# Performance work log

Measured on AMD Instinct MI355X. Metric: run time of the kernel, lower is better.

Reference implementation:

```python
import jax, jax.numpy as jnp
import numpy as np
import math

B, S, D, NPOS = 8, 2048, 768, 512


def setup_inputs() -> dict:
    key = jax.random.key(0)
    ks = jax.random.split(key, 9)
    std = 0.02
    return {
        "token_embeddings": jax.random.normal(ks[0], (B, S, D), dtype=jnp.float32),
        "attention_mask": jnp.ones((B, S), dtype=jnp.int32),
        "Wq": jax.random.normal(ks[1], (D, D), dtype=jnp.float32) * std,
        "bq": jax.random.normal(ks[2], (D,), dtype=jnp.float32) * std,
        "Wk": jax.random.normal(ks[3], (D, D), dtype=jnp.float32) * std,
        "bk": jax.random.normal(ks[4], (D,), dtype=jnp.float32) * std,
        "Wv": jax.random.normal(ks[5], (D, D), dtype=jnp.float32) * std,
        "bv": jax.random.normal(ks[6], (D,), dtype=jnp.float32) * std,
        "pos_emb": jax.random.normal(ks[7], (D, NPOS), dtype=jnp.float32) * std,
    }


def reference(token_embeddings, attention_mask, Wq, bq, Wk, bk, Wv, bv, pos_emb):
    scale = 1.0 / math.sqrt(D)
    q = token_embeddings @ Wq.T + bq  # [B,S,D]
    k = token_embeddings @ Wk.T + bk
    v = token_embeddings @ Wv.T + bv

    logits = jnp.einsum("bsd,btd->bst", q, k) * scale  # [B,S,S]
    logits = jnp.where(attention_mask[:, None, :] == 0, -jnp.inf, logits)

    # CoPE: gate-based fractional positions + interpolated learned bias
    gates = jax.nn.sigmoid(logits)
    pos = jnp.flip(jnp.cumsum(jnp.flip(gates, -1), axis=-1), -1)  # reverse cumsum
    pos = jnp.minimum(pos, float(NPOS - 1))
    pos_floor = jnp.floor(pos)
    pos_ceil = jnp.ceil(pos)
    logits_int = jnp.einsum("bsd,dn->bsn", q, pos_emb)  # [B,S,NPOS]
    lc = jnp.take_along_axis(logits_int, pos_ceil.astype(jnp.int32), axis=-1)
    lf = jnp.take_along_axis(logits_int, pos_floor.astype(jnp.int32), axis=-1)
    w = pos - pos_floor
    logits = logits + lc * w + lf * (1.0 - w)

    attn = jax.nn.softmax(logits, axis=-1)
    out = jnp.einsum("bst,btd->bsd", attn, v)
    return out[:, 0, :]  # CLS pooled sentence embedding [B,D]
```

## Files before the change

kernel.cpp:

```cpp
#include <hip/hip_runtime.h>
#include <hip/hip_bf16.h>
#include <math.h>

#define BB 8
#define SS 2048
#define DD 768
#define NPOS 512
#define TC 64
#define DSPLIT 16
#define DSL (DD / DSPLIT)
#define ETOT (DD + NPOS)
#define SCALE 0.036084391824351615f

#define WS_LOGITS 0
#define WS_CTX    16384
#define WS_Q      22528
#define WS_PWS    28672
#define WS_PWQ    192512

__device__ __forceinline__ float wave_sum(float v) {
    #pragma unroll
    for (int off = 32; off > 0; off >>= 1) v += __shfl_xor(v, off, 64);
    return v;
}

__global__ __launch_bounds__(256) void k_q(const float* __restrict__ x,
        const float* __restrict__ Wq, const float* __restrict__ bq,
        float* __restrict__ q, float* __restrict__ ctx) {
    int zi = blockIdx.x * 256 + threadIdx.x;
    if (zi < BB * DD) ctx[zi] = 0.f;
    int gw = zi >> 6;
    int lane = threadIdx.x & 63;
    if (gw >= BB * DD) return;
    int b = gw / DD, d = gw % DD;
    const float4* vr = (const float4*)(x + (size_t)b * SS * DD);
    const float4* wr = (const float4*)(Wq + (size_t)d * DD);
    float acc = 0.f;
    #pragma unroll
    for (int j = 0; j < 3; ++j) {
        float4 a = vr[lane + 64 * j];
        float4 w = wr[lane + 64 * j];
        acc += a.x * w.x + a.y * w.y + a.z * w.z + a.w * w.w;
    }
    acc = wave_sum(acc);
    if (lane == 0) q[gw] = acc + bq[d];
}

__global__ __launch_bounds__(256) void k_qkw(const float* __restrict__ q,
        const float* __restrict__ Wk, const float* __restrict__ bk,
        const float* __restrict__ pos_emb,
        float* __restrict__ pws, float* __restrict__ pwq) {
    int part = blockIdx.x, ds = blockIdx.y, tid = threadIdx.x;
    __shared__ float qs[BB][DSL];
    for (int i = tid; i < BB * DSL; i += 256) {
        int b = i / DSL, d = i % DSL;
        qs[b][d] = q[b * DD + ds * DSL + d];
    }
    __syncthreads();
    const float* Wsrc; int stride, eg;
    if (part < 3) { Wsrc = Wk; stride = DD; eg = part * 256 + tid; }
    else { Wsrc = pos_emb; stride = NPOS; eg = DD + (part - 3) * 256 + tid; }
    int e = (part < 3) ? eg : eg - DD;
    const float* col = Wsrc + (size_t)(ds * DSL) * stride + e;
    float acc[BB];
    #pragma unroll
    for (int b = 0; b < BB; ++b) acc[b] = 0.f;
    #pragma unroll 4
    for (int d = 0; d < DSL; ++d) {
        float w = col[(size_t)d * stride];
        #pragma unroll
        for (int b = 0; b < BB; ++b) acc[b] += qs[b][d] * w;
    }
    #pragma unroll
    for (int b = 0; b < BB; ++b)
        pws[((size_t)ds * BB + b) * ETOT + eg] = acc[b];
    if (part == 0 && tid < BB) {
        float p = 0.f;
        #pragma unroll
        for (int d = 0; d < DSL; ++d) p += qs[tid][d] * bk[ds * DSL + d];
        pwq[ds * BB + tid] = p;
    }
}

__global__ __launch_bounds__(1024) void k_logits(const float* __restrict__ x,
        const float* __restrict__ pws, const float* __restrict__ pwq,
        const int* __restrict__ mask, float* __restrict__ logits) {
    const int chunk = blockIdx.x, b = blockIdx.y, tid = threadIdx.x;
    const int lane = tid & 63, wid = tid >> 6;
    __shared__ float sq[4][192];
    __shared__ float sqbk;
    if (tid < DD) {
        float acc = 0.f;
        #pragma unroll 4
        for (int ds = 0; ds < DSPLIT; ++ds)
            acc += pws[((size_t)ds * BB + b) * ETOT + tid];
        sq[tid & 3][tid >> 2] = acc;
    }
    if (wid == 15) {
        float p = (lane < DSPLIT) ? pwq[lane * BB + b] : 0.f;
        p = wave_sum(p);
        if (lane == 0) sqbk = p;
    }
    __syncthreads();
    #pragma unroll 2
    for (int r = 0; r < 8; ++r) {
        int trow = chunk * 128 + wid * 8 + r;
        const float4* xr = (const float4*)(x + ((size_t)b * SS + trow) * DD);
        float acc = 0.f;
        #pragma unroll
        for (int j = 0; j < 3; ++j) {
            int i = lane + 64 * j;
            float4 a = xr[i];
            acc += a.x * sq[0][i] + a.y * sq[1][i] + a.z * sq[2][i] + a.w * sq[3][i];
        }
        acc = wave_sum(acc);
        if (lane == 0) {
            int o = b * SS + trow;
            logits[o] = mask[o] ? (acc + sqbk) * SCALE : -INFINITY;
        }
    }
}

__global__ __launch_bounds__(256) void k_ctxscan(const float* __restrict__ x,
        const float* __restrict__ logits, const float* __restrict__ pws,
        float* __restrict__ ctx) {
    const int tc = blockIdx.x, b = blockIdx.y, tid = threadIdx.x;
    __shared__ float lg[SS];
    __shared__ float li[NPOS];
    __shared__ float sa[256], sb[256];
    for (int i = tid; i < SS; i += 256) lg[i] = logits[b * SS + i];
    for (int e = tid; e < NPOS; e += 256) {
        float acc = 0.f;
        #pragma unroll 4
        for (int ds = 0; ds < DSPLIT; ++ds)
            acc += pws[((size_t)ds * BB + b) * ETOT + DD + e];
        li[e] = acc;
    }
    __syncthreads();
    int base = tid * 8;
    float loc[8];
    float run = 0.f;
    #pragma unroll
    for (int k = 7; k >= 0; --k) {
        float v = lg[base + k];
        float gk = 1.f / (1.f + expf(-v));
        run += gk;
        loc[k] = run;
    }
    sa[tid] = run;
    __syncthreads();
    float* src = sa; float* dst = sb;
    for (int off = 1; off < 256; off <<= 1) {
        float v = src[tid];
        if (tid + off < 256) v += src[tid + off];
        dst[tid] = v;
        __syncthreads();
        float* t_ = src; src = dst; dst = t_;
    }
    float st = (tid < 255) ? src[tid + 1] : 0.f;
    float adj[8];
    float m = -INFINITY;
    #pragma unroll
    for (int k = 0; k < 8; ++k) {
        float val = lg[base + k];
        float nv;
        if (val == -INFINITY) {
            nv = val;
        } else {
            float p = fminf(loc[k] + st, (float)(NPOS - 1));
            float pf = floorf(p);
            float wt = p - pf;
            int fi = (int)pf;
            int ci = (int)ceilf(p);
            nv = val + li[ci] * wt + li[fi] * (1.f - wt);
        }
        adj[k] = nv;
        m = fmaxf(m, nv);
    }
    __syncthreads();
    sa[tid] = m;
    __syncthreads();
    for (int s2 = 128; s2 > 0; s2 >>= 1) {
        if (tid < s2) sa[tid] = fmaxf(sa[tid], sa[tid + s2]);
        __syncthreads();
    }
    float bm = sa[0];
    __syncthreads();
    float sum = 0.f;
    #pragma unroll
    for (int k = 0; k < 8; ++k) { adj[k] = expf(adj[k] - bm); sum += adj[k]; }
    sa[tid] = sum;
    __syncthreads();
    for (int s2 = 128; s2 > 0; s2 >>= 1) {
        if (tid < s2) sa[tid] += sa[tid + s2];
        __syncthreads();
    }
    float inv = 1.f / sa[0];
    #pragma unroll
    for (int k = 0; k < 8; ++k) lg[base + k] = adj[k] * inv;
    __syncthreads();
    if (tid < 192) {
        const int TPC = SS / TC;
        float4 acc = make_float4(0.f, 0.f, 0.f, 0.f);
        const float4* xr = (const float4*)(x + ((size_t)b * SS + (size_t)tc * TPC) * DD);
        const float* at = lg + tc * TPC;
        for (int i = 0; i < TPC; ++i) {
            float a = at[i];
            float4 xv = xr[(size_t)i * 192 + tid];
            acc.x += a * xv.x; acc.y += a * xv.y; acc.z += a * xv.z; acc.w += a * xv.w;
        }
        float* dstp = ctx + b * DD + tid * 4;
        atomicAdd(dstp + 0, acc.x);
        atomicAdd(dstp + 1, acc.y);
        atomicAdd(dstp + 2, acc.z);
        atomicAdd(dstp + 3, acc.w);
    }
}

__global__ __launch_bounds__(256) void k_out(const float* __restrict__ ctx,
        const float* __restrict__ Wv, const float* __restrict__ bv,
        float* __restrict__ out) {
    int gw = (blockIdx.x * 256 + threadIdx.x) >> 6;
    int lane = threadIdx.x & 63;
    if (gw >= BB * DD) return;
    int b = gw / DD, d = gw % DD;
    const float4* vr = (const float4*)(ctx + (size_t)b * DD);
    const float4* wr = (const float4*)(Wv + (size_t)d * DD);
    float acc = 0.f;
    #pragma unroll
    for (int j = 0; j < 3; ++j) {
        float4 a = vr[lane + 64 * j];
        float4 w = wr[lane + 64 * j];
        acc += a.x * w.x + a.y * w.y + a.z * w.z + a.w * w.w;
    }
    acc = wave_sum(acc);
    if (lane == 0) out[gw] = acc + bv[d];
}

extern "C" void kernel_launch(void* const* d_in, const int* in_sizes, int n_in,
                              void* d_out, int out_size, void* d_ws, size_t ws_size,
                              hipStream_t stream) {
    const float* x       = (const float*)d_in[0];
    const int*   mask    = (const int*)  d_in[1];
    const float* Wq      = (const float*)d_in[2];
    const float* bq      = (const float*)d_in[3];
    const float* Wk      = (const float*)d_in[4];
    const float* bk      = (const float*)d_in[5];
    const float* Wv      = (const float*)d_in[6];
    const float* bv      = (const float*)d_in[7];
    const float* pos_emb = (const float*)d_in[8];
    float* out = (float*)d_out;
    float* ws  = (float*)d_ws;

    float* logits = ws + WS_LOGITS;
    float* ctx    = ws + WS_CTX;
    float* q      = ws + WS_Q;
    float* pws    = ws + WS_PWS;
    float* pwq    = ws + WS_PWQ;

    k_q<<<dim3((BB * DD) / 4), dim3(256), 0, stream>>>(x, Wq, bq, q, ctx);
    k_qkw<<<dim3(5, DSPLIT), dim3(256), 0, stream>>>(q, Wk, bk, pos_emb, pws, pwq);
    k_logits<<<dim3(16, BB), dim3(1024), 0, stream>>>(x, pws, pwq, mask, logits);
    k_ctxscan<<<dim3(TC, BB), dim3(256), 0, stream>>>(x, logits, pws, ctx);
    k_out<<<dim3((BB * DD) / 4), dim3(256), 0, stream>>>(ctx, Wv, bv, out);
}
```

Baseline: 53.90 us.

## Split partial-sum reduction into separate kernel and flatten logits to one wave per row

Adds a small reduction kernel that sums the DSPLIT partial products once into qk and positional-logit buffers. Previously every logits block and every ctxscan block re-reduced them. k_logits now uses 256-thread blocks with one wave per token row across 4096 blocks, instead of 128 blocks of 1024 threads each looping over 8 rows. The q·bk bias term is now computed in a single block. The cost is one extra kernel launch and a round trip through global memory.

```diff
diff --git a/kernel.cpp b/kernel.cpp
--- a/kernel.cpp
+++ b/kernel.cpp
@@ -15,8 +15,10 @@
 #define WS_LOGITS 0
 #define WS_CTX    16384
 #define WS_Q      22528
-#define WS_PWS    28672
-#define WS_PWQ    192512
+#define WS_QK     28672
+#define WS_LI     34816
+#define WS_QBK    38912
+#define WS_PWS    38928
 
 __device__ __forceinline__ float wave_sum(float v) {
     #pragma unroll
@@ -49,7 +51,7 @@
 __global__ __launch_bounds__(256) void k_qkw(const float* __restrict__ q,
         const float* __restrict__ Wk, const float* __restrict__ bk,
         const float* __restrict__ pos_emb,
-        float* __restrict__ pws, float* __restrict__ pwq) {
+        float* __restrict__ pws, float* __restrict__ qbk) {
     int part = blockIdx.x, ds = blockIdx.y, tid = threadIdx.x;
     __shared__ float qs[BB][DSL];
     for (int i = tid; i < BB * DSL; i += 256) {
@@ -74,68 +76,66 @@
     #pragma unroll
     for (int b = 0; b < BB; ++b)
         pws[((size_t)ds * BB + b) * ETOT + eg] = acc[b];
-    if (part == 0 && tid < BB) {
-        float p = 0.f;
+    if (part == 0 && ds == 0) {
+        int w = tid >> 6, lane = tid & 63;
         #pragma unroll
-        for (int d = 0; d < DSL; ++d) p += qs[tid][d] * bk[ds * DSL + d];
-        pwq[ds * BB + tid] = p;
-    }
-}
-
-__global__ __launch_bounds__(1024) void k_logits(const float* __restrict__ x,
-        const float* __restrict__ pws, const float* __restrict__ pwq,
+        for (int r = 0; r < 2; ++r) {
+            int b = w + 4 * r;
+            float p = 0.f;
+            #pragma unroll
+            for (int j = 0; j < 12; ++j)
+                p += q[b * DD + lane + 64 * j] * bk[lane + 64 * j];
+            p = wave_sum(p);
+            if (lane == 0) qbk[b] = p;
+        }
+    }
+}
+
+__global__ __launch_bounds__(256) void k_qkr(const float* __restrict__ pws,
+        float* __restrict__ qk, float* __restrict__ lint) {
+    int idx = blockIdx.x * 256 + threadIdx.x;
+    if (idx >= BB * ETOT) return;
+    int b = idx / ETOT, e = idx % ETOT;
+    float acc = 0.f;
+    #pragma unroll
+    for (int ds = 0; ds < DSPLIT; ++ds)
+        acc += pws[((size_t)ds * BB + b) * ETOT + e];
+    if (e < DD) qk[b * DD + e] = acc;
+    else lint[b * NPOS + (e - DD)] = acc;
+}
+
+__global__ __launch_bounds__(256) void k_logits(const float* __restrict__ x,
+        const float* __restrict__ qk, const float* __restrict__ qbk,
         const int* __restrict__ mask, float* __restrict__ logits) {
-    const int chunk = blockIdx.x, b = blockIdx.y, tid = threadIdx.x;
-    const int lane = tid & 63, wid = tid >> 6;
-    __shared__ float sq[4][192];
-    __shared__ float sqbk;
-    if (tid < DD) {
-        float acc = 0.f;
-        #pragma unroll 4
-        for (int ds = 0; ds < DSPLIT; ++ds)
-            acc += pws[((size_t)ds * BB + b) * ETOT + tid];
-        sq[tid & 3][tid >> 2] = acc;
-    }
-    if (wid == 15) {
-        float p = (lane < DSPLIT) ? pwq[lane * BB + b] : 0.f;
-        p = wave_sum(p);
-        if (lane == 0) sqbk = p;
-    }
-    __syncthreads();
-    #pragma unroll 2
-    for (int r = 0; r < 8; ++r) {
-        int trow = chunk * 128 + wid * 8 + r;
-        const float4* xr = (const float4*)(x + ((size_t)b * SS + trow) * DD);
-        float acc = 0.f;
-        #pragma unroll
-        for (int j = 0; j < 3; ++j) {
-            int i = lane + 64 * j;
-            float4 a = xr[i];
-            acc += a.x * sq[0][i] + a.y * sq[1][i] + a.z * sq[2][i] + a.w * sq[3][i];
-        }
-        acc = wave_sum(acc);
-        if (lane == 0) {
-            int o = b * SS + trow;
-            logits[o] = mask[o] ? (acc + sqbk) * SCALE : -INFINITY;
-        }
+    int gw = (blockIdx.x * 256 + threadIdx.x) >> 6;
+    int lane = threadIdx.x & 63;
+    if (gw >= BB * SS) return;
+    int b = gw >> 11;
+    const float4* xr = (const float4*)(x + (size_t)gw * DD);
+    const float4* wr = (const float4*)(qk + (size_t)b * DD);
+    float acc = 0.f;
+    #pragma unroll
+    for (int j = 0; j < 3; ++j) {
+        float4 a = xr[lane + 64 * j];
+        float4 w = wr[lane + 64 * j];
+        acc += a.x * w.x + a.y * w.y + a.z * w.z + a.w * w.w;
+    }
+    acc = wave_sum(acc);
+    if (lane == 0) {
+        float lg = (acc + qbk[b]) * SCALE;
+        logits[gw] = mask[gw] ? lg : -INFINITY;
     }
 }
 
 __global__ __launch_bounds__(256) void k_ctxscan(const float* __restrict__ x,
-        const float* __restrict__ logits, const float* __restrict__ pws,
+        const float* __restrict__ logits, const float* __restrict__ lint,
         float* __restrict__ ctx) {
     const int tc = blockIdx.x, b = blockIdx.y, tid = threadIdx.x;
     __shared__ float lg[SS];
     __shared__ float li[NPOS];
     __shared__ float sa[256], sb[256];
     for (int i = tid; i < SS; i += 256) lg[i] = logits[b * SS + i];
-    for (int e = tid; e < NPOS; e += 256) {
-        float acc = 0.f;
-        #pragma unroll 4
-        for (int ds = 0; ds < DSPLIT; ++ds)
-            acc += pws[((size_t)ds * BB + b) * ETOT + DD + e];
-        li[e] = acc;
-    }
+    for (int i = tid; i < NPOS; i += 256) li[i] = lint[b * NPOS + i];
     __syncthreads();
     int base = tid * 8;
     float loc[8];
@@ -255,12 +255,15 @@
     float* logits = ws + WS_LOGITS;
     float* ctx    = ws + WS_CTX;
     float* q      = ws + WS_Q;
+    float* qk     = ws + WS_QK;
+    float* lint   = ws + WS_LI;
+    float* qbk    = ws + WS_QBK;
     float* pws    = ws + WS_PWS;
-    float* pwq    = ws + WS_PWQ;
 
     k_q<<<dim3((BB * DD) / 4), dim3(256), 0, stream>>>(x, Wq, bq, q, ctx);
-    k_qkw<<<dim3(5, DSPLIT), dim3(256), 0, stream>>>(q, Wk, bk, pos_emb, pws, pwq);
-    k_logits<<<dim3(16, BB), dim3(1024), 0, stream>>>(x, pws, pwq, mask, logits);
-    k_ctxscan<<<dim3(TC, BB), dim3(256), 0, stream>>>(x, logits, pws, ctx);
+    k_qkw<<<dim3(5, DSPLIT), dim3(256), 0, stream>>>(q, Wk, bk, pos_emb, pws, qbk);
+    k_qkr<<<dim3(40), dim3(256), 0, stream>>>(pws, qk, lint);
+    k_logits<<<dim3((BB * SS) / 4), dim3(256), 0, stream>>>(x, qk, qbk, mask, logits);
+    k_ctxscan<<<dim3(TC, BB), dim3(256), 0, stream>>>(x, logits, lint, ctx);
     k_out<<<dim3((BB * DD) / 4), dim3(256), 0, stream>>>(ctx, Wv, bv, out);
 }
```

New measurement: 51.18 us. -5.0%, faster.
